# Kernel tuning notes

Measured on AMD Instinct MI355X. Metric: run time of the kernel, lower is better.

## Reference

```python
import jax, jax.numpy as jnp
import numpy as np

K = 256
Q = 64
T = 500001  # length of return series r


def setup_inputs() -> dict:
    key = jax.random.key(0)
    k_r, k_b, k_w0, k_w = jax.random.split(key, 4)
    r = 0.01 * jax.random.normal(k_r, (T,), dtype=jnp.float32)
    a0 = jnp.float32(0.0)
    a1 = jnp.float32(0.0)
    raw_beta0 = jnp.float32(-4.0)
    raw_beta = (-4.0 + 0.1 * jax.random.normal(k_b, (K,))).astype(jnp.float32)
    raw_w0 = (-8.0 + 0.1 * jax.random.normal(k_w0, (K,))).astype(jnp.float32)
    raw_w = (-4.0 + 0.1 * jax.random.normal(k_w, (K, Q))).astype(jnp.float32)
    return {"r": r, "a0": a0, "a1": a1, "raw_beta0": raw_beta0,
            "raw_beta": raw_beta, "raw_w0": raw_w0, "raw_w": raw_w}


def reference(r, a0, a1, raw_beta0, raw_beta, raw_w0, raw_w):
    # AR(1) residuals
    u = r[1:] - a0 - a1 * r[:-1]          # [T-1]
    u2 = u * u                            # [T-1]
    n = u.shape[0]
    # init_u2 = unbiased variance of u2, repeated q times (torch.var default ddof=1)
    init_u2 = jnp.full((Q,), jnp.var(u2, ddof=1), dtype=u2.dtype)
    u2_full = jnp.concatenate([init_u2, u2])  # [q + T-1]
    # vectorized windowing: row t holds u2_full[t+q-1], ..., u2_full[t] (flipped window)
    t_idx = jnp.arange(n)[:, None]        # [n,1]
    lag_idx = jnp.arange(Q)[None, :]      # [1,q]
    idx = (Q + t_idx) - 1 - lag_idx       # [n,q]
    u2_lags = u2_full[idx]                # [n,q]
    # softplus-MLP volatility
    w0 = jax.nn.softplus(raw_w0)          # [k]
    w = jax.nn.softplus(raw_w)            # [k,q]
    h = jax.nn.relu(w0[None, :] + u2_lags @ w.T)  # [n,k]
    beta0 = jax.nn.softplus(raw_beta0)
    beta = jax.nn.softplus(raw_beta)      # [k]
    sigma2 = beta0 + h @ beta + 1e-8      # [n]
    # Gaussian negative log-likelihood
    nll = (0.5 * n * jnp.log(jnp.float32(2.0 * np.pi))
           + 0.5 * jnp.sum(jnp.log(sigma2))
           + 0.5 * jnp.sum(u2 / sigma2))
    return nll
```

## Files before the change

kernel.cpp:

```cpp
#include <hip/hip_runtime.h>
#include <math.h>

#define K_ 256
#define Q_ 64
#define NT 500000
#define NTILES (NT / 16)
#define TT_ 32
#define GRID_MAIN ((NTILES + TT_ - 1) / TT_)
#define NSUM 245

#define WS_BETA0  2
#define WS_U2B0   4
#define U2ELEMS   (Q_ + NT + 16)
#define U2F       ((U2ELEMS + 1) / 2)
#define WS_U2B1   (WS_U2B0 + U2F)
#define WS_BPACK  (WS_U2B1 + U2F)
#define WS_W0     (WS_BPACK + 8192)
#define WS_BETA   (WS_W0 + K_)
#define WS_PART   (WS_BETA + K_)
#define WS_PART2  (WS_PART + 512)
#define WS_OUT    (WS_PART2 + 512)
#define WS_CNT    (WS_OUT + 1024)

typedef __attribute__((ext_vector_type(8))) __bf16 bf16x8;
typedef __attribute__((ext_vector_type(4))) float  f32x4;

__device__ __forceinline__ float softplusf(float x) {
    return (x > 20.f) ? x : log1pf(__expf(x));
}

__device__ __forceinline__ unsigned short f2bf(float f) {
    unsigned int u = __float_as_uint(f);
    u = u + 0x7FFFu + ((u >> 16) & 1u);
    return (unsigned short)(u >> 16);
}

__global__ void k_sum(const float* __restrict__ r,
                      const float* __restrict__ a0p,
                      const float* __restrict__ a1p,
                      float* __restrict__ ws) {
    __shared__ float red[8];
    int i0 = (blockIdx.x * 256 + threadIdx.x) * 8;
    float a0 = a0p[0], a1 = a1p[0];
    float v = 0.f, v2 = 0.f;
    if (i0 < NT) {
        float rr[9];
        *(float4*)&rr[0] = *(const float4*)(r + i0);
        *(float4*)&rr[4] = *(const float4*)(r + i0 + 4);
        rr[8] = r[i0 + 8];
        unsigned short bs[8];
        #pragma unroll
        for (int j = 0; j < 8; ++j) {
            float u  = rr[j + 1] - a0 - a1 * rr[j];
            float u2 = u * u;
            bs[j] = f2bf(u2);
            v += u2;
            v2 = fmaf(u2, u2, v2);
        }
        unsigned short* b0 = (unsigned short*)(ws + WS_U2B0);
        unsigned short* b1 = (unsigned short*)(ws + WS_U2B1);
        __builtin_memcpy(b0 + Q_ + i0, bs, 16);
        b1[Q_ - 1 + i0] = bs[0];
        __builtin_memcpy(b1 + Q_ + i0, bs + 1, 12);
        b1[Q_ + i0 + 6] = bs[7];
    }
    #pragma unroll
    for (int off = 32; off > 0; off >>= 1) {
        v  += __shfl_down(v,  off, 64);
        v2 += __shfl_down(v2, off, 64);
    }
    int wv = threadIdx.x >> 6;
    if ((threadIdx.x & 63) == 0) { red[wv * 2] = v; red[wv * 2 + 1] = v2; }
    __syncthreads();
    if (threadIdx.x == 0) {
        ws[WS_PART  + blockIdx.x] = red[0] + red[2] + red[4] + red[6];
        ws[WS_PART2 + blockIdx.x] = red[1] + red[3] + red[5] + red[7];
    }
}

__global__ void k_prep(const float* __restrict__ raw_beta0,
                       const float* __restrict__ raw_beta,
                       const float* __restrict__ raw_w0,
                       const float* __restrict__ raw_w,
                       float* __restrict__ ws) {
    int idx = blockIdx.x * blockDim.x + threadIdx.x;
    if (idx < 16384) {
        int jj = idx & 7, l = (idx >> 3) & 63, s = (idx >> 9) & 1, kc = idx >> 10;
        int j    = 32 * s + 8 * (l >> 4) + jj;
        int kout = kc * 16 + (l & 15);
        ((unsigned short*)(ws + WS_BPACK))[idx] =
            f2bf(softplusf(raw_w[kout * Q_ + (Q_ - 1 - j)]));
    } else if (idx < 16384 + K_) {
        int k = idx - 16384;
        ws[WS_W0 + k] = softplusf(raw_w0[k]);
    } else if (idx < 16384 + 2 * K_) {
        int k = idx - (16384 + K_);
        ws[WS_BETA + k] = softplusf(raw_beta[k]);
    } else if (idx < 16384 + 2 * K_ + Q_) {
        int j = idx - (16384 + 2 * K_);
        float s1 = 0.f, s2 = 0.f;
        #pragma unroll
        for (int p = j; p < NSUM; p += 64) {
            s1 += ws[WS_PART  + p];
            s2 += ws[WS_PART2 + p];
        }
        #pragma unroll
        for (int mask = 1; mask < 64; mask <<= 1) {
            s1 += __shfl_xor(s1, mask, 64);
            s2 += __shfl_xor(s2, mask, 64);
        }
        float n  = (float)NT;
        float var = (s2 - s1 * s1 / n) / (n - 1.f);
        unsigned short b = f2bf(var);
        ((unsigned short*)(ws + WS_U2B0))[j] = b;
        if (j < Q_ - 1) ((unsigned short*)(ws + WS_U2B1))[j] = b;
        if (j == 0) ws[WS_BETA0] = softplusf(raw_beta0[0]);
    }
}

__launch_bounds__(256, 4)
__global__ void k_main(const float* __restrict__ r,
                       const float* __restrict__ a0p,
                       const float* __restrict__ a1p,
                       float* __restrict__ ws, float* __restrict__ out) {
    __shared__ __align__(16) float sig[TT_ * 256];
    __shared__ float red[4];
    __shared__ int lastflag;

    int tid = threadIdx.x;
    int l = tid & 63, w = tid >> 6;
    int m = l & 15, q = l >> 4;

    const unsigned short* bp = (const unsigned short*)(ws + WS_BPACK);
    float beta0v = ws[WS_BETA0];
    float a0 = a0p[0], a1 = a1p[0];

    bf16x8 Wf[4][2];
    f32x4 w0c[4], betc[4];
    #pragma unroll
    for (int i = 0; i < 4; ++i) {
        int kc = w * 4 + i;
        #pragma unroll
        for (int s = 0; s < 2; ++s)
            __builtin_memcpy(&Wf[i][s], bp + ((kc * 2 + s) * 64 + l) * 8, 16);
        w0c[i]  = *(const f32x4*)(ws + WS_W0   + kc * 16 + q * 4);
        betc[i] = *(const f32x4*)(ws + WS_BETA + kc * 16 + q * 4);
    }

    int par = m & 1;
    const char* abase = (const char*)(ws + (par ? WS_U2B1 : WS_U2B0));
    int aoff = (blockIdx.x * 512 + m + 8 * q - par) * 2;

    bf16x8 U0, U1, U0n, U1n;
    __builtin_memcpy(&U0, abase + aoff, 16);
    __builtin_memcpy(&U1, abase + aoff + 64, 16);

    #pragma unroll 2
    for (int it = 0; it < TT_; ++it) {
        int anext = aoff + 32;
        __builtin_memcpy(&U0n, abase + anext, 16);
        __builtin_memcpy(&U1n, abase + anext + 64, 16);

        float p[4];
        #pragma unroll
        for (int i = 0; i < 4; ++i) {
            f32x4 acc = __builtin_amdgcn_mfma_f32_16x16x32_bf16(Wf[i][0], U0, w0c[i], 0, 0, 0);
            acc = __builtin_amdgcn_mfma_f32_16x16x32_bf16(Wf[i][1], U1, acc, 0, 0, 0);
            float pi;
            pi = betc[i][0] * fmaxf(acc[0], 0.f);
            pi = fmaf(betc[i][1], fmaxf(acc[1], 0.f), pi);
            pi = fmaf(betc[i][2], fmaxf(acc[2], 0.f), pi);
            pi = fmaf(betc[i][3], fmaxf(acc[3], 0.f), pi);
            p[i] = pi;
        }
        sig[it * 256 + tid] = (p[0] + p[1]) + (p[2] + p[3]);

        aoff = anext; U0 = U0n; U1 = U1n;
    }

    __syncthreads();

    float val = 0.f;
    #pragma unroll
    for (int rep = 0; rep < 2; ++rep) {
        int lt = tid + rep * 256;
        int tile = lt >> 4, tt = lt & 15;
        const float* sp = &sig[tile * 256 + tt];
        float s = 0.f;
        #pragma unroll
        for (int wq = 0; wq < 16; ++wq) s += sp[wq * 16];
        float sg = beta0v + s + 1e-8f;
        int t = blockIdx.x * 512 + lt;
        if (t < NT) {
            float u  = r[t + 1] - a0 - a1 * r[t];
            val += __logf(sg) + (u * u) / sg;
        }
    }
    #pragma unroll
    for (int mask = 1; mask < 64; mask <<= 1)
        val += __shfl_xor(val, mask, 64);
    if (l == 0) red[w] = val;
    __syncthreads();

    if (tid == 0) {
        ws[WS_OUT + blockIdx.x] = red[0] + red[1] + red[2] + red[3];
        __threadfence();
        unsigned old = atomicAdd((unsigned*)(ws + WS_CNT), 1u);
        lastflag = (old == GRID_MAIN - 1);
    }
    __syncthreads();
    if (lastflag) {
        __threadfence();
        float s = 0.f;
        for (int p = tid; p < GRID_MAIN; p += 256) s += ws[WS_OUT + p];
        #pragma unroll
        for (int mask = 1; mask < 64; mask <<= 1)
            s += __shfl_xor(s, mask, 64);
        if (l == 0) red[w] = s;
        __syncthreads();
        if (tid == 0)
            out[0] = 0.5f * (float)NT * 1.8378770664093453f
                   + 0.5f * (red[0] + red[1] + red[2] + red[3]);
    }
}

extern "C" void kernel_launch(void* const* d_in, const int* in_sizes, int n_in,
                              void* d_out, int out_size, void* d_ws, size_t ws_size,
                              hipStream_t stream) {
    const float* r        = (const float*)d_in[0];
    const float* a0       = (const float*)d_in[1];
    const float* a1       = (const float*)d_in[2];
    const float* raw_b0   = (const float*)d_in[3];
    const float* raw_beta = (const float*)d_in[4];
    const float* raw_w0   = (const float*)d_in[5];
    const float* raw_w    = (const float*)d_in[6];
    float* out = (float*)d_out;
    float* ws  = (float*)d_ws;

    hipMemsetAsync(ws + WS_CNT, 0, 4, stream);

    k_sum<<<NSUM, 256, 0, stream>>>(r, a0, a1, ws);

    int prep_threads = 16384 + 2 * K_ + Q_;
    k_prep<<<(prep_threads + 255) / 256, 256, 0, stream>>>(
        raw_b0, raw_beta, raw_w0, raw_w, ws);

    k_main<<<GRID_MAIN, 256, 0, stream>>>(r, a0, a1, ws, out);
}
```

Measured before the change: 107.3 us.

## Stage weights and input window in LDS, halve per-block time tiles

Each block now cooperatively copies the packed bf16 weight matrix, w0, beta and its u2 window into shared memory, then reads the MFMA operands from LDS instead of issuing per-lane global loads. TT_ drops from 32 to 16, doubling the grid to about 1954 blocks with 256 timesteps each, and the end-of-block reduction becomes one step per thread. The launch-bounds occupancy hint is removed. The aim is to replace scattered global/L2 traffic with LDS reads and spread the work over more blocks, at the cost of about 41 KB of LDS per block, which limits resident blocks per CU, and twice as many per-block weight loads and atomics.

Result: slower. 125.6 us (+17.1%).

```diff
diff --git a/kernel.cpp b/kernel.cpp
--- a/kernel.cpp
+++ b/kernel.cpp
@@ -5,7 +5,7 @@
 #define Q_ 64
 #define NT 500000
 #define NTILES (NT / 16)
-#define TT_ 32
+#define TT_ 16
 #define GRID_MAIN ((NTILES + TT_ - 1) / TT_)
 #define NSUM 245
 
@@ -20,7 +20,7 @@
 #define WS_PART   (WS_BETA + K_)
 #define WS_PART2  (WS_PART + 512)
 #define WS_OUT    (WS_PART2 + 512)
-#define WS_CNT    (WS_OUT + 1024)
+#define WS_CNT    (WS_OUT + 2048)
 
 typedef __attribute__((ext_vector_type(8))) __bf16 bf16x8;
 typedef __attribute__((ext_vector_type(4))) float  f32x4;
@@ -118,11 +118,15 @@
     }
 }
 
-__launch_bounds__(256, 4)
+__launch_bounds__(256)
 __global__ void k_main(const float* __restrict__ r,
                        const float* __restrict__ a0p,
                        const float* __restrict__ a1p,
                        float* __restrict__ ws, float* __restrict__ out) {
+    __shared__ __align__(16) unsigned short Wlds[16384];
+    __shared__ __align__(16) unsigned short Ulds[2][320];
+    __shared__ __align__(16) float w0lds[K_];
+    __shared__ __align__(16) float betlds[K_];
     __shared__ __align__(16) float sig[TT_ * 256];
     __shared__ float red[4];
     __shared__ int lastflag;
@@ -130,11 +134,31 @@
     int tid = threadIdx.x;
     int l = tid & 63, w = tid >> 6;
     int m = l & 15, q = l >> 4;
-
-    const unsigned short* bp = (const unsigned short*)(ws + WS_BPACK);
+    int t0g = blockIdx.x * 256;
+
     float beta0v = ws[WS_BETA0];
     float a0 = a0p[0], a1 = a1p[0];
 
+    {
+        const uint4* wg = (const uint4*)(ws + WS_BPACK);
+        uint4* wl = (uint4*)Wlds;
+        #pragma unroll
+        for (int i = 0; i < 8; ++i) wl[tid + 256 * i] = wg[tid + 256 * i];
+
+        if (tid < 40) {
+            const uint4* ug = (const uint4*)((const unsigned short*)(ws + WS_U2B0) + t0g);
+            ((uint4*)&Ulds[0][0])[tid] = ug[tid];
+        } else if (tid < 80) {
+            const uint4* ug = (const uint4*)((const unsigned short*)(ws + WS_U2B1) + t0g);
+            ((uint4*)&Ulds[1][0])[tid - 40] = ug[tid - 40];
+        } else if (tid < 144) {
+            ((uint4*)w0lds)[tid - 80] = ((const uint4*)(ws + WS_W0))[tid - 80];
+        } else if (tid < 208) {
+            ((uint4*)betlds)[tid - 144] = ((const uint4*)(ws + WS_BETA))[tid - 144];
+        }
+    }
+    __syncthreads();
+
     bf16x8 Wf[4][2];
     f32x4 w0c[4], betc[4];
     #pragma unroll
@@ -142,24 +166,21 @@
         int kc = w * 4 + i;
         #pragma unroll
         for (int s = 0; s < 2; ++s)
-            __builtin_memcpy(&Wf[i][s], bp + ((kc * 2 + s) * 64 + l) * 8, 16);
-        w0c[i]  = *(const f32x4*)(ws + WS_W0   + kc * 16 + q * 4);
-        betc[i] = *(const f32x4*)(ws + WS_BETA + kc * 16 + q * 4);
+            __builtin_memcpy(&Wf[i][s], Wlds + ((kc * 2 + s) * 64 + l) * 8, 16);
+        w0c[i]  = *(const f32x4*)(w0lds  + kc * 16 + q * 4);
+        betc[i] = *(const f32x4*)(betlds + kc * 16 + q * 4);
     }
 
     int par = m & 1;
-    const char* abase = (const char*)(ws + (par ? WS_U2B1 : WS_U2B0));
-    int aoff = (blockIdx.x * 512 + m + 8 * q - par) * 2;
-
-    bf16x8 U0, U1, U0n, U1n;
-    __builtin_memcpy(&U0, abase + aoff, 16);
-    __builtin_memcpy(&U1, abase + aoff + 64, 16);
-
-    #pragma unroll 2
+    int ubase = par * 320 + (m + 8 * q - par);
+    const unsigned int* uflat = (const unsigned int*)&Ulds[0][0];
+
+    #pragma unroll 4
     for (int it = 0; it < TT_; ++it) {
-        int anext = aoff + 32;
-        __builtin_memcpy(&U0n, abase + anext, 16);
-        __builtin_memcpy(&U1n, abase + anext + 64, 16);
+        const unsigned int* up = uflat + ((ubase + 16 * it) >> 1);
+        bf16x8 U0, U1;
+        __builtin_memcpy(&U0, up, 16);
+        __builtin_memcpy(&U1, up + 16, 16);
 
         float p[4];
         #pragma unroll
@@ -174,27 +195,21 @@
             p[i] = pi;
         }
         sig[it * 256 + tid] = (p[0] + p[1]) + (p[2] + p[3]);
-
-        aoff = anext; U0 = U0n; U1 = U1n;
-    }
-
-    __syncthreads();
-
+    }
+
+    __syncthreads();
+
+    int tile = tid >> 4, tt = tid & 15;
+    const float* sp = &sig[tile * 256 + tt];
+    float s = 0.f;
+    #pragma unroll
+    for (int c = 0; c < 16; ++c) s += sp[c * 16];
+    float sg = beta0v + s + 1e-8f;
+    int t = t0g + tid;
     float val = 0.f;
-    #pragma unroll
-    for (int rep = 0; rep < 2; ++rep) {
-        int lt = tid + rep * 256;
-        int tile = lt >> 4, tt = lt & 15;
-        const float* sp = &sig[tile * 256 + tt];
-        float s = 0.f;
-        #pragma unroll
-        for (int wq = 0; wq < 16; ++wq) s += sp[wq * 16];
-        float sg = beta0v + s + 1e-8f;
-        int t = blockIdx.x * 512 + lt;
-        if (t < NT) {
-            float u  = r[t + 1] - a0 - a1 * r[t];
-            val += __logf(sg) + (u * u) / sg;
-        }
+    if (t < NT) {
+        float u = r[t + 1] - a0 - a1 * r[t];
+        val = __logf(sg) + (u * u) / sg;
     }
     #pragma unroll
     for (int mask = 1; mask < 64; mask <<= 1)
@@ -203,7 +218,7 @@
     __syncthreads();
 
     if (tid == 0) {
-        ws[WS_OUT + blockIdx.x] = red[0] + red[1] + red[2] + red[3];
+        ws[WS_OUT + blockIdx.x] = (red[0] + red[1]) + (red[2] + red[3]);
         __threadfence();
         unsigned old = atomicAdd((unsigned*)(ws + WS_CNT), 1u);
         lastflag = (old == GRID_MAIN - 1);
@@ -211,16 +226,16 @@
     __syncthreads();
     if (lastflag) {
         __threadfence();
-        float s = 0.f;
-        for (int p = tid; p < GRID_MAIN; p += 256) s += ws[WS_OUT + p];
+        float s2 = 0.f;
+        for (int p = tid; p < GRID_MAIN; p += 256) s2 += ws[WS_OUT + p];
         #pragma unroll
         for (int mask = 1; mask < 64; mask <<= 1)
-            s += __shfl_xor(s, mask, 64);
-        if (l == 0) red[w] = s;
+            s2 += __shfl_xor(s2, mask, 64);
+        if (l == 0) red[w] = s2;
         __syncthreads();
         if (tid == 0)
             out[0] = 0.5f * (float)NT * 1.8378770664093453f
-                   + 0.5f * (red[0] + red[1] + red[2] + red[3]);
+                   + 0.5f * ((red[0] + red[1]) + (red[2] + red[3]));
     }
 }
 
```
